# Kernel tuning notes

Hardware: AMD Instinct MI355X
Metric: run time of the kernel (lower is better)

## Reference

```python
import jax, jax.numpy as jnp
import numpy as np

T, B, E, H = 64, 64, 128, 256
N_ITEMS, N_DATA = 50000, 20000
EPS = 1e-8


def setup_inputs() -> dict:
    key = jax.random.key(0)
    ks = jax.random.split(key, 20)
    lengths = jnp.sort(jax.random.randint(ks[0], (B,), 1, T + 1))[::-1]
    lengths = lengths.at[0].set(T)  # pack_padded_sequence expects max length first
    x = jax.random.randint(ks[1], (T, B), 1, N_ITEMS)
    tmask = jnp.arange(T)[:, None] < lengths[None, :]
    x = jnp.where(tmask, x, 0)  # padding index 0
    s = 0.05
    emb_table = (jax.random.normal(ks[2], (N_ITEMS, E)) * s).at[0].set(0.0)  # padding_idx=0
    data_embeddings = jax.random.normal(ks[3], (N_DATA, E)) * s
    return {
        'x': x, 'lengths': lengths,
        'emb_table': emb_table, 'data_embeddings': data_embeddings,
        'W_ih': jax.random.normal(ks[4], (4 * H, E)) * s,
        'W_hh': jax.random.normal(ks[5], (4 * H, H)) * s,
        'b_ih': jax.random.normal(ks[6], (4 * H,)) * s,
        'b_hh': jax.random.normal(ks[7], (4 * H,)) * s,
        'Wq': jax.random.normal(ks[8], (H, H)) * s, 'bq': jax.random.normal(ks[9], (H,)) * s,
        'Wk': jax.random.normal(ks[10], (H, H)) * s, 'bk': jax.random.normal(ks[11], (H,)) * s,
        'Wv': jax.random.normal(ks[12], (H, H)) * s, 'bv': jax.random.normal(ks[13], (H,)) * s,
        'W_out': jax.random.normal(ks[14], (E, H)) * s, 'b_out': jax.random.normal(ks[15], (E,)) * s,
    }


def _forward(x, lengths, emb_table, data_embeddings, W_ih, W_hh, b_ih, b_hh,
             Wq, bq, Wk, bk, Wv, bv, W_out, b_out):
    t_len, b_sz = x.shape
    e_dim = emb_table.shape[1]
    h_dim = W_hh.shape[1]

    embs0 = emb_table[x]  # (T, B, E); dropout is identity in eval mode
    initial_embs = jax.lax.stop_gradient(embs0)  # .clone().detach() in original

    # PositionalEncoding: original slices by x.size(1) == batch dim (faithful quirk)
    pos = jnp.arange(b_sz, dtype=jnp.float32)[:, None]
    div = jnp.exp(jnp.arange(0, e_dim, 2, dtype=jnp.float32) * (-jnp.log(10000.0) / e_dim))
    enc = jnp.stack([jnp.sin(pos * div), jnp.cos(pos * div)], axis=-1).reshape(b_sz, e_dim)
    embs = embs0 + enc[None, :, :]  # broadcast over time

    # single-layer LSTM over time (gate order i, f, g, o)
    def step(carry, x_t):
        h, c = carry
        gates = x_t @ W_ih.T + h @ W_hh.T + (b_ih + b_hh)  # (B, 4H)
        i, f, g, o = jnp.split(gates, 4, axis=-1)
        c = jax.nn.sigmoid(f) * c + jax.nn.sigmoid(i) * jnp.tanh(g)
        h = jax.nn.sigmoid(o) * jnp.tanh(c)
        return (h, c), h

    h0 = jnp.zeros((b_sz, h_dim), embs.dtype)
    (_, _), lstm_out = jax.lax.scan(step, (h0, h0), embs)  # (T, B, H)

    # pack/pad round-trip zeroes outputs past each length (LSTM is causal)
    tmask = jnp.arange(t_len)[:, None] < lengths[None, :]  # (T, B)
    lstm_out = lstm_out * tmask[:, :, None]
    lstm_out = lstm_out.transpose(1, 0, 2)  # (B, T, H)

    padding_mask = jnp.sum(lstm_out, axis=-1) != 0  # (B, T)

    q = lstm_out @ Wq.T + bq
    k = lstm_out @ Wk.T + bk
    v = lstm_out @ Wv.T + bv
    score = jnp.einsum('bth,bsh->bts', q, k) / jnp.sqrt(jnp.float32(h_dim))
    score = jnp.where(padding_mask[:, None, :], score, -jnp.inf)
    attn = jax.nn.softmax(score, axis=2)
    weighted = jnp.einsum('bts,bsh->bth', attn, v)  # (B, T, H)
    attn_output = jnp.mean(weighted, axis=1) @ W_out.T + b_out  # (B, E)

    # kNN: fused normalize + matmul + argmin + gather over all T at once
    qn = initial_embs / jnp.clip(jnp.linalg.norm(initial_embs, axis=-1, keepdims=True), EPS)
    dn = data_embeddings / jnp.clip(jnp.linalg.norm(data_embeddings, axis=-1, keepdims=True), EPS)
    sims = jnp.einsum('tbe,ne->tbn', qn, dn)  # (T, B, N_DATA)
    idx = jnp.argmax(sims, axis=-1)  # argmin of (1 - sim)
    closest = jnp.mean(data_embeddings[idx], axis=0)  # (B, E)

    attn_output = attn_output * closest
    return attn_output @ emb_table.T  # (B, n_items)


def reference(x, lengths, emb_table, data_embeddings, W_ih, W_hh, b_ih, b_hh,
              Wq, bq, Wk, bk, Wv, bv, W_out, b_out):
    return _forward(x, lengths, emb_table, data_embeddings, W_ih, W_hh, b_ih, b_hh,
                    Wq, bq, Wk, bk, Wv, bv, W_out, b_out)
```

## Files before the change

### kernel.cpp

```cpp
#include <hip/hip_runtime.h>

typedef unsigned int uint;
typedef unsigned short ushort;
typedef unsigned long long u64;

#define NITEMS 50000
#define NDATA  20000
#define BLKCAP 4096u
#define OVCAP  65536u

#define OFF_LSTMOUT   0x0000000ULL
#define OFF_HX        0x0400000ULL
#define OFF_HXM       0x0440000ULL
#define OFF_PACKED    0x0480000ULL
#define OFF_PACKED2   0x0488000ULL
#define OFF_HITCNTS   0x0490000ULL
#define OFF_OHITCNT   0x0490800ULL
#define MEMSET_BYTES  0x0491000ULL
#define OFF_QMARGIN   0x0491000ULL
#define OFF_XW        0x05A0000ULL
#define OFF_QKV       0x15A0000ULL
#define OFF_HITBUF    OFF_QKV
#define OFF_WIHT      0x21A0000ULL
#define OFF_WQKVT     0x2220000ULL
#define OFF_BIASIH    0x22E0000ULL
#define OFF_BQKV      0x22E1000ULL
#define OFF_DNSCALE   0x22E2000ULL
#define OFF_AV        0x22FE000ULL
#define OFF_DEMB16    0x2306000ULL
#define OFF_A16       0x27E8000ULL
#define OFF_OVF       0x28E8000ULL

__device__ __forceinline__ ushort f2bf(float f) {
  union { float f; uint u; } v; v.f = f;
  uint u = v.u;
  return (ushort)((u + 0x7FFFu + ((u >> 16) & 1u)) >> 16);
}
__device__ __forceinline__ uint fkey(float f) {
  union { float f; uint u; } v; v.f = f;
  return (v.u & 0x80000000u) ? ~v.u : (v.u | 0x80000000u);
}
__device__ __forceinline__ u64 shfl_xor_u64(u64 v, int off) {
  uint lo = (uint)v, hi = (uint)(v >> 32);
  lo = (uint)__shfl_xor((int)lo, off);
  hi = (uint)__shfl_xor((int)hi, off);
  return ((u64)hi << 32) | (u64)lo;
}

typedef __attribute__((ext_vector_type(8))) short short8;
typedef __attribute__((ext_vector_type(4))) float floatx4;

#define R32(M) M(0) M(1) M(2) M(3) M(4) M(5) M(6) M(7) M(8) M(9) M(10) M(11) \
  M(12) M(13) M(14) M(15) M(16) M(17) M(18) M(19) M(20) M(21) M(22) M(23) \
  M(24) M(25) M(26) M(27) M(28) M(29) M(30) M(31)

#define HIX(j) ((j) + (((j) >> 7) << 2))

#define LBAR() do { \
  __builtin_amdgcn_sched_barrier(0); \
  asm volatile("s_waitcnt lgkmcnt(0)" ::: "memory"); \
  __builtin_amdgcn_s_barrier(); \
  __builtin_amdgcn_sched_barrier(0); \
} while (0)

__global__ __launch_bounds__(256) void prep_kernel(
    const int* __restrict__ x,
    const float* __restrict__ emb, const float* __restrict__ demb,
    const float* __restrict__ W_ih,
    const float* __restrict__ Wq, const float* __restrict__ Wk, const float* __restrict__ Wv,
    const float* __restrict__ b_ih, const float* __restrict__ b_hh,
    const float* __restrict__ bq, const float* __restrict__ bk, const float* __restrict__ bv,
    float* __restrict__ dnscale, ushort* __restrict__ demb16, ushort* __restrict__ a16,
    float* __restrict__ wiht, float* __restrict__ wqkvt,
    float* __restrict__ biasih, float* __restrict__ bqkv,
    float* __restrict__ qmargin, u64* __restrict__ packed2)
{
  int blk = blockIdx.x, tid = threadIdx.x;
  if (blk < 5000) {
    int row = blk * 4 + (tid >> 6);
    int lane = tid & 63;
    float2 d = *(const float2*)(demb + (size_t)row * 128 + lane * 2);
    float s = d.x * d.x + d.y * d.y;
    for (int off = 32; off; off >>= 1) s += __shfl_xor(s, off);
    if (lane == 0) dnscale[row] = 1.0f / fmaxf(sqrtf(s), 1e-8f);
  } else if (blk < 6250) {
    size_t base = ((size_t)(blk - 5000) * 256 + tid) * 8;
    float4 f1 = *(const float4*)(demb + base);
    float4 f2 = *(const float4*)(demb + base + 4);
    uint4 o;
    o.x = (uint)f2bf(f1.x) | ((uint)f2bf(f1.y) << 16);
    o.y = (uint)f2bf(f1.z) | ((uint)f2bf(f1.w) << 16);
    o.z = (uint)f2bf(f2.x) | ((uint)f2bf(f2.y) << 16);
    o.w = (uint)f2bf(f2.z) | ((uint)f2bf(f2.w) << 16);
    *(uint4*)(demb16 + base) = o;
  } else if (blk < 6506) {
    int idx = (blk - 6250) * 256 + tid;
    int m = idx >> 4, seg = idx & 15;
    const float* src = emb + (size_t)x[m] * 128 + seg * 8;
    float4 f1 = *(const float4*)(src);
    float4 f2 = *(const float4*)(src + 4);
    uint4 o;
    o.x = (uint)f2bf(f1.x) | ((uint)f2bf(f1.y) << 16);
    o.y = (uint)f2bf(f1.z) | ((uint)f2bf(f1.w) << 16);
    o.z = (uint)f2bf(f2.x) | ((uint)f2bf(f2.y) << 16);
    o.w = (uint)f2bf(f2.z) | ((uint)f2bf(f2.w) << 16);
    *(uint4*)(a16 + (size_t)m * 128 + seg * 8) = o;
  } else if (blk < 7018) {
    int f = (blk - 6506) * 256 + tid;
    int r = f >> 7, e = f & 127;
    wiht[e * 1024 + r] = W_ih[f];
  } else if (blk < 7786) {
    int f = (blk - 7018) * 256 + tid;
    int w = f >> 16; int rem = f & 65535;
    int r = rem >> 8, e = rem & 255;
    const float* src = (w == 0) ? Wq : (w == 1) ? Wk : Wv;
    wqkvt[e * 768 + w * 256 + r] = src[rem];
  } else if (blk < 7790) {
    int idx = (blk - 7786) * 256 + tid;
    if (idx < 1024) biasih[idx] = b_ih[idx] + b_hh[idx];
  } else if (blk < 7793) {
    int idx = (blk - 7790) * 256 + tid;
    if (idx < 768) {
      int w = idx >> 8; int r = idx & 255;
      const float* src = (w == 0) ? bq : (w == 1) ? bk : bv;
      bqkv[idx] = src[r];
    }
  } else {
    int row = (blk - 7793) * 4 + (tid >> 6);
    int lane = tid & 63;
    float2 d = *(const float2*)(emb + (size_t)x[row] * 128 + lane * 2);
    float s = d.x * d.x + d.y * d.y;
    for (int off = 32; off; off >>= 1) s += __shfl_xor(s, off);
    if (lane == 0) {
      if (s == 0.f) {
        qmargin[row] = -1e30f;
        packed2[row] = ((u64)fkey(0.0f) << 32) | 0xFFFFFFFFull;
      } else {
        qmargin[row] = 0.017f * sqrtf(s) + 1e-5f;
      }
    }
  }
}

__global__ __launch_bounds__(256) void xw_kernel(
    const int* __restrict__ x, const float* __restrict__ emb,
    const float* __restrict__ wiht, const float* __restrict__ biasih,
    float* __restrict__ xW)
{
  __shared__ __align__(16) float At[128 * 16];
  int blk = blockIdx.x, tid = threadIdx.x;
  int m0 = blk * 16;
  for (int c = 0; c < 8; ++c) {
    int idx = c * 256 + tid;
    int mm = idx >> 7, e = idx & 127;
    int m = m0 + mm;
    int bcol = m & 63;
    int xv = x[m];
    float val = emb[(size_t)xv * 128 + e];
    int j = e >> 1;
    float arg = (float)bcol * __expf((float)j * -0.14391157f);
    val += (e & 1) ? cosf(arg) : sinf(arg);
    At[e * 16 + mm] = val;
  }
  __syncthreads();
  int quad = tid >> 6, l = tid & 63;
  for (int rp = 0; rp < 4; ++rp) {
    int r = rp * 256 + l * 4;
    float acc[4][4] = {};
    for (int e = 0; e < 128; ++e) {
      float4 wv4 = *(const float4*)(wiht + e * 1024 + r);
      float4 av4 = *(const float4*)(At + e * 16 + quad * 4);
      float am[4] = {av4.x, av4.y, av4.z, av4.w};
      float wr4[4] = {wv4.x, wv4.y, wv4.z, wv4.w};
      #pragma unroll
      for (int mi = 0; mi < 4; ++mi)
        #pragma unroll
        for (int ri = 0; ri < 4; ++ri)
          acc[mi][ri] += am[mi] * wr4[ri];
    }
    float4 bv4 = *(const float4*)(biasih + r);
    #pragma unroll
    for (int mi = 0; mi < 4; ++mi) {
      size_t m = (size_t)(m0 + quad * 4 + mi);
      float4 o;
      o.x = acc[mi][0] + bv4.x; o.y = acc[mi][1] + bv4.y;
      o.z = acc[mi][2] + bv4.z; o.w = acc[mi][3] + bv4.w;
      *(float4*)(xW + m * 1024 + r) = o;
    }
  }
}

__global__ __launch_bounds__(512, 2) void lstm_knn_kernel(
    const int* __restrict__ lengths, const float* __restrict__ Whh,
    const float* __restrict__ xW, float* __restrict__ lstm_out,
    u64* __restrict__ hx, u64* __restrict__ hxm,
    const ushort* __restrict__ a16, const ushort* __restrict__ demb16,
    const float* __restrict__ dnscale, const float* __restrict__ qmargin,
    u64* __restrict__ packed, uint* __restrict__ hitcnts, uint* __restrict__ ohitcnt,
    uint* __restrict__ hitbuf, uint* __restrict__ ovbuf,
    const int* __restrict__ x, const float* __restrict__ emb,
    const float* __restrict__ demb, u64* __restrict__ packed2)
{
  __shared__ __align__(16) float h_sh[264];
  __shared__ float part_sh[256];
  __shared__ __align__(16) ushort b_sh[2][64 * 144];
  __shared__ uint lcnt;
  int tid = threadIdx.x;

  if (blockIdx.x < 256) {
    int blk = blockIdx.x;
    int b = blk & 63, q = blk >> 6;
    int row_local = tid >> 1, half = tid & 1;
    int gate = row_local >> 6, jloc = row_local & 63;
    int grow = gate * 256 + q * 64 + jloc;
    const float4* wp4 = (const float4*)(Whh + (size_t)grow * 256 + half * 128);
#define WDECL(i) float4 tt##i = wp4[i]; \
  float w##i##x = tt##i.x, w##i##y = tt##i.y, w##i##z = tt##i.z, w##i##w = tt##i.w;
    R32(WDECL)
#define WPIN(i) asm volatile("" : "+v"(w##i##x), "+v"(w##i##y), "+v"(w##i##z), "+v"(w##i##w));
    R32(WPIN)
    int len = lengths[b];
    if (tid < 256) h_sh[HIX(tid)] = 0.f;
    float cval = 0.f;
    int prm = tid - 320;
    int jr = (prm < q * 64) ? prm : prm + 64;
    bool fast_ok = true;
    int j1 = q * 64 + (tid - 64);
    float xw0 = 0.f, xw1 = 0.f, xw2 = 0.f, xw3 = 0.f;
    if (tid < 64) {
      const float* xwrow = xW + ((size_t)0 * 64 + b) * 1024 + q * 64 + tid;
      xw0 = xwrow[0]; xw1 = xwrow[256]; xw2 = xwrow[512]; xw3 = xwrow[768];
    }
    __syncthreads();
    for (int t = 0; t < len; ++t) {
      float nx0 = 0.f, nx1 = 0.f, nx2 = 0.f, nx3 = 0.f;
      if (tid < 64 && t + 1 < len) {
        const float* xwrow = xW + ((size_t)(t + 1) * 64 + b) * 1024 + q * 64 + tid;
        nx0 = xwrow[0]; nx1 = xwrow[256]; nx2 = xwrow[512]; nx3 = xwrow[768];
      }
      float hprev = 0.f;
      if (tid >= 64 && tid < 128 && t > 0) hprev = h_sh[HIX(j1)];
      const float4* h4 = (const float4*)(h_sh + half * 132);
      float a[4] = {0.f, 0.f, 0.f, 0.f};
#define WACC(i) { float4 hv_ = h4[i]; \
    a[(i) & 3] += w##i##x * hv_.x + w##i##y * hv_.y + w##i##z * hv_.z + w##i##w * hv_.w; }
      R32(WACC)
      float acc = (a[0] + a[2]) + (a[1] + a[3]);
      acc += __shfl_xor(acc, 1);
      if (!half) part_sh[row_local] = acc;
      LBAR();
      if (tid < 64) {
        float gi = part_sh[tid]       + xw0;
        float gf = part_sh[64 + tid]  + xw1;
        float gg = part_sh[128 + tid] + xw2;
        float go = part_sh[192 + tid] + xw3;
        float ii = 1.f / (1.f + __expf(-gi));
        float ff = 1.f / (1.f + __expf(-gf));
        float oo = 1.f / (1.f + __expf(-go));
        float tg = 1.f - 2.f / (1.f + __expf(2.f * gg));
        cval = ff * cval + ii * tg;
        float tc = 1.f - 2.f / (1.f + __expf(2.f * cval));
        float hv = oo * tc;
        int j = q * 64 + tid;
        union { float f; uint u; } cu; cu.f = hv;
        u64 pk = ((u64)cu.u << 32) | (u64)(uint)(t + 1);
        size_t slot = ((size_t)((t + 1) & 1) * 64 + b) * 256 + j;
        __builtin_amdgcn_sched_barrier(0);
        asm volatile("s_waitcnt vmcnt(4)" ::: "memory");
        asm volatile("global_store_dwordx2 %0, %1, off"
                     :: "v"(hxm + slot), "v"(pk) : "memory");
        __hip_atomic_store(hx + slot, pk, __ATOMIC_RELAXED, __HIP_MEMORY_SCOPE_AGENT);
        h_sh[HIX(j)] = hv;
        xw0 = nx0; xw1 = nx1; xw2 = nx2; xw3 = nx3;
      } else if (tid < 128) {
        if (t > 0) lstm_out[((size_t)b * 64 + (t - 1)) * 256 + j1] = hprev;
      } else if (tid >= 320 && t + 1 < len) {
        size_t slot = ((size_t)((t + 1) & 1) * 64 + b) * 256 + jr;
        uint want = (uint)(t + 1);
        u64 v = 0;
        bool got = false;
        if (fast_ok) {
          const u64* ms = hxm + slot;
          for (int tries = 0; tries < 32; ++tries) {
            asm volatile("global_load_dwordx2 %0, %1, off sc0\n\t"
                         "s_waitcnt vmcnt(0)"
                         : "=&v"(v) : "v"(ms) : "memory");
            if ((uint)v == want) { got = true; break; }
          }
          if (!got && t > 0) fast_ok = false;
        }
        if (!got) {
          const u64* as = hx + slot;
          int guard = 0;
          while (true) {
            v = __hip_atomic_load(as, __ATOMIC_RELAXED, __HIP_MEMORY_SCOPE_AGENT);
            if ((uint)v == want || ++guard > (1 << 24)) break;
          }
        }
        union { uint u; float f; } cv; cv.u = (uint)(v >> 32);
        h_sh[HIX(jr)] = cv.f;
      }
      LBAR();
    }
    if (tid >= 64 && tid < 128) {
      float hl = h_sh[HIX(j1)];
      lstm_out[((size_t)b * 64 + (len - 1)) * 256 + j1] = hl;
    }
    return;
  }

  int kb = blockIdx.x - 256;
  int chunk = kb & 15, mt = kb >> 4;
  int w8 = tid >> 6;
  int s = w8 >> 2, wv2 = w8 & 3;
  int lane = tid & 63;
  int col = lane & 15, quad = lane >> 4;
  int M0 = mt * 128;
  if (tid == 0) lcnt = 0;
  short8 afrag[4];
  {
    int mrow = M0 + s * 64 + wv2 * 16 + col;
    #pragma unroll
    for (int kf = 0; kf < 4; ++kf)
      afrag[kf] = *(const short8*)(a16 + (size_t)mrow * 128 + kf * 32 + quad * 8);
  }
  float best[4] = {-1e30f, -1e30f, -1e30f, -1e30f};
  int bidx[4] = {};
  int nbase = chunk * 1250, nend = nbase + 1250;
  const int niter = 20;
  int srow = tid >> 4, sseg = tid & 15;
  uint4 stg[2]; float scr[4];

  #pragma unroll
  for (int p = 0; p < 2; ++p) {
    int n = nbase + p * 32 + srow;
    uint4 v = {0u,0u,0u,0u};
    if (n < nend) v = *(const uint4*)(demb16 + (size_t)n * 128 + sseg * 8);
    stg[p] = v;
  }
  #pragma unroll
  for (int ns = 0; ns < 4; ++ns) {
    int n = nbase + ns * 16 + col;
    scr[ns] = (n < nend) ? dnscale[n] : 0.f;
  }
  for (int it = 0; it < niter; ++it) {
    int n0 = nbase + it * 64;
    ushort* bsh = b_sh[it & 1];
    #pragma unroll
    for (int p = 0; p < 2; ++p)
      *(uint4*)(&bsh[(p * 32 + srow) * 144 + sseg * 8]) = stg[p];
    float mysc[4] = {scr[0], scr[1], scr[2], scr[3]};
    __syncthreads();
    if (it + 1 < niter) {
      int nb = n0 + 64;
      #pragma unroll
      for (int p = 0; p < 2; ++p) {
        int n = nb + p * 32 + srow;
        uint4 v = {0u,0u,0u,0u};
        if (n < nend) v = *(const uint4*)(demb16 + (size_t)n * 128 + sseg * 8);
        stg[p] = v;
      }
      #pragma unroll
      for (int ns = 0; ns < 4; ++ns) {
        int n = nb + ns * 16 + col;
        scr[ns] = (n < nend) ? dnscale[n] : 0.f;
      }
    }
    #pragma unroll
    for (int ns = 0; ns < 4; ++ns) {
      short8 bfr[4];
      #pragma unroll
      for (int kf = 0; kf < 4; ++kf)
        bfr[kf] = *(const short8*)(&bsh[(ns * 16 + col) * 144 + kf * 32 + quad * 8]);
      int n = n0 + ns * 16 + col;
      float sc = mysc[ns];
      bool valid = (n < nend);
      floatx4 acc = {0.f, 0.f, 0.f, 0.f};
      #pragma unroll
      for (int kf = 0; kf < 4; ++kf)
        acc = __builtin_amdgcn_mfma_f32_16x16x32_bf16(afrag[kf], bfr[kf], acc, 0, 0, 0);
      #pragma unroll
      for (int r = 0; r < 4; ++r) {
        float sim = acc[r] * sc;
        if (valid && sim > best[r]) { best[r] = sim; bidx[r] = n; }
      }
    }
  }
  float thr[4];
  #pragma unroll
  for (int r = 0; r < 4; ++r) {
    u64 p = ((u64)fkey(best[r]) << 32) | (u64)(0xFFFFFFFFu - (uint)bidx[r]);
    #pragma unroll
    for (int off = 1; off < 16; off <<= 1) {
      u64 o = shfl_xor_u64(p, off);
      if (o > p) p = o;
    }
    int m = M0 + s * 64 + wv2 * 16 + quad * 4 + r;
    union { uint u; float f; } bu;
    uint k = (uint)(p >> 32);
    bu.u = (k & 0x80000000u) ? (k & 0x7FFFFFFFu) : ~k;
    thr[r] = bu.f - qmargin[m];
    if (col == 0)
      atomicMax((unsigned long long*)&packed[m], (unsigned long long)p);
  }
  __syncthreads();

  uint* myregion = hitbuf + (size_t)kb * BLKCAP;
  uint* ovregion = ovbuf;
  #pragma unroll
  for (int p = 0; p < 2; ++p) {
    int n = nbase + p * 32 + srow;
    uint4 v = {0u,0u,0u,0u};
    if (n < nend) v = *(const uint4*)(demb16 + (size_t)n * 128 + sseg * 8);
    stg[p] = v;
  }
  #pragma unroll
  for (int ns = 0; ns < 4; ++ns) {
    int n = nbase + ns * 16 + col;
    scr[ns] = (n < nend) ? dnscale[n] : 0.f;
  }
  for (int it = 0; it < niter; ++it) {
    int n0 = nbase + it * 64;
    ushort* bsh = b_sh[it & 1];
    #pragma unroll
    for (int p = 0; p < 2; ++p)
      *(uint4*)(&bsh[(p * 32 + srow) * 144 + sseg * 8]) = stg[p];
    float mysc[4] = {scr[0], scr[1], scr[2], scr[3]};
    __syncthreads();
    if (it + 1 < niter) {
      int nb = n0 + 64;
      #pragma unroll
      for (int p = 0; p < 2; ++p) {
        int n = nb + p * 32 + srow;
        uint4 v = {0u,0u,0u,0u};
        if (n < nend) v = *(const uint4*)(demb16 + (size_t)n * 128 + sseg * 8);
        stg[p] = v;
      }
      #pragma unroll
      for (int ns = 0; ns < 4; ++ns) {
        int n = nb + ns * 16 + col;
        scr[ns] = (n < nend) ? dnscale[n] : 0.f;
      }
    }
    #pragma unroll
    for (int ns = 0; ns < 4; ++ns) {
      short8 bfr[4];
      #pragma unroll
      for (int kf = 0; kf < 4; ++kf)
        bfr[kf] = *(const short8*)(&bsh[(ns * 16 + col) * 144 + kf * 32 + quad * 8]);
      int n = n0 + ns * 16 + col;
      float sc = mysc[ns];
      bool valid = (n < nend);
      floatx4 acc = {0.f, 0.f, 0.f, 0.f};
      #pragma unroll
      for (int kf = 0; kf < 4; ++kf)
        acc = __builtin_amdgcn_mfma_f32_16x16x32_bf16(afrag[kf], bfr[kf], acc, 0, 0, 0);
      #pragma unroll
      for (int r = 0; r < 4; ++r) {
        float sim = acc[r] * sc;
        bool hit = valid && (sim >= thr[r]);
        u64 mask = __ballot(hit);
        if (mask) {
          uint lcntv = (uint)__popcll(mask);
          int leader = __ffsll((unsigned long long)mask) - 1;
          uint base = 0;
          if (lane == leader) base = atomicAdd(&lcnt, lcntv);
          base = (uint)__shfl((int)base, leader);
          if (hit) {
            uint pos = base + (uint)__popcll(mask & ((1ull << lane) - 1ull));
            uint mm = (uint)(M0 + s * 64 + wv2 * 16 + quad * 4 + r);
            uint rec = (mm << 15) | (uint)n;
            if (pos < BLKCAP) {
              myregion[pos] = rec;
            } else {
              uint op = atomicAdd(ohitcnt, 1u);
              if (op < OVCAP) ovregion[op] = rec;
            }
          }
        }
      }
    }
  }
  __syncthreads();
  if (tid == 0) hitcnts[kb] = lcnt;
  uint rcnt = lcnt; if (rcnt > BLKCAP) rcnt = BLKCAP;
  for (uint h = tid; h < rcnt; h += 512) {
    uint rec = myregion[h];
    uint m = rec >> 15, n = rec & 0x7FFFu;
    if (m >= 4096 || n >= NDATA) continue;
    const float* qr = emb + (size_t)x[m] * 128;
    const float* dr = demb + (size_t)n * 128;
    double p = 0.0;
    #pragma unroll 8
    for (int e = 0; e < 128; e += 2) {
      float2 qv = *(const float2*)(qr + e);
      float2 dv = *(const float2*)(dr + e);
      p += (double)qv.x * (double)dv.x + (double)qv.y * (double)dv.y;
    }
    float sx = (float)(p * (double)dnscale[n]);
    u64 key = ((u64)fkey(sx) << 32) | (u64)(0xFFFFFFFFu - n);
    atomicMax((unsigned long long*)&packed2[m], (unsigned long long)key);
  }
}

__global__ __launch_bounds__(256) void fused_post_kernel(
    const float* __restrict__ lstm_out, const float* __restrict__ wqkvt,
    const float* __restrict__ bqkv, float* __restrict__ qkv,
    const u64* __restrict__ packed, const uint* __restrict__ ohitcnt,
    const uint* __restrict__ ovbuf, const int* __restrict__ x,
    const float* __restrict__ emb, const float* __restrict__ demb,
    const float* __restrict__ dnscale, u64* __restrict__ packed2)
{
  __shared__ __align__(16) float At[256 * 16];
  int blk = blockIdx.x, tid = threadIdx.x;
  if (blk < 256) {
    int m0 = blk * 16;
    for (int c = 0; c < 16; ++c)
      At[tid * 16 + c] = lstm_out[((size_t)m0 + c) * 256 + tid];
    __syncthreads();
    int quad = tid >> 6, l = tid & 63;
    for (int rp = 0; rp < 3; ++rp) {
      int r = rp * 256 + l * 4;
      float acc[4][4] = {};
      for (int e = 0; e < 256; ++e) {
        float4 wv4 = *(const float4*)(wqkvt + (size_t)e * 768 + r);
        float4 av4 = *(const float4*)(At + e * 16 + quad * 4);
        float am[4] = {av4.x, av4.y, av4.z, av4.w};
        float wr4[4] = {wv4.x, wv4.y, wv4.z, wv4.w};
        #pragma unroll
        for (int mi = 0; mi < 4; ++mi)
          #pragma unroll
          for (int ri = 0; ri < 4; ++ri)
            acc[mi][ri] += am[mi] * wr4[ri];
      }
      float4 bv4 = *(const float4*)(bqkv + r);
      #pragma unroll
      for (int mi = 0; mi < 4; ++mi) {
        size_t m = (size_t)(m0 + quad * 4 + mi);
        float4 o;
        o.x = acc[mi][0] + bv4.x; o.y = acc[mi][1] + bv4.y;
        o.z = acc[mi][2] + bv4.z; o.w = acc[mi][3] + bv4.w;
        *(float4*)(qkv + m * 768 + r) = o;
      }
    }
    return;
  }
  if (blk < 272) {
    uint m = (uint)(blk - 256) * 256 + tid;
    uint n = 0xFFFFFFFFu - (uint)(packed[m] & 0xFFFFFFFFull);
    if (n < NDATA) {
      const float* qr = emb + (size_t)x[m] * 128;
      const float* dr = demb + (size_t)n * 128;
      double p = 0.0;
      #pragma unroll 8
      for (int e = 0; e < 128; e += 2) {
        float2 qv = *(const float2*)(qr + e);
        float2 dv = *(const float2*)(dr + e);
        p += (double)qv.x * (double)dv.x + (double)qv.y * (double)dv.y;
      }
      float sx = (float)(p * (double)dnscale[n]);
      u64 key = ((u64)fkey(sx) << 32) | (u64)(0xFFFFFFFFu - n);
      atomicMax((unsigned long long*)&packed2[m], (unsigned long long)key);
    }
    return;
  }
  uint cnt = *ohitcnt; if (cnt > OVCAP) cnt = OVCAP;
  for (uint h = (uint)(blk - 272) * 256 + tid; h < cnt; h += 16 * 256) {
    uint rec = ovbuf[h];
    uint m = rec >> 15, n = rec & 0x7FFFu;
    if (m >= 4096 || n >= NDATA) continue;
    const float* qr = emb + (size_t)x[m] * 128;
    const float* dr = demb + (size_t)n * 128;
    double p = 0.0;
    #pragma unroll 8
    for (int e = 0; e < 128; e += 2) {
      float2 qv = *(const float2*)(qr + e);
      float2 dv = *(const float2*)(dr + e);
      p += (double)qv.x * (double)dv.x + (double)qv.y * (double)dv.y;
    }
    float sx = (float)(p * (double)dnscale[n]);
    u64 key = ((u64)fkey(sx) << 32) | (u64)(0xFFFFFFFFu - n);
    atomicMax((unsigned long long*)&packed2[m], (unsigned long long)key);
  }
}

__global__ __launch_bounds__(256) void attn_kernel(
    const float* __restrict__ qkv, const int* __restrict__ lengths,
    const u64* __restrict__ packed2, const float* __restrict__ demb,
    const float* __restrict__ W_out, const float* __restrict__ b_out,
    float* __restrict__ av)
{
  __shared__ float k_sh[64 * 257];
  __shared__ __align__(16) float q_sh[4 * 256];
  __shared__ float wpart[4 * 64];
  __shared__ float wtot[64];
  __shared__ float out_sh[256];
  int b = blockIdx.x, tid = threadIdx.x;
  int wv = tid >> 6, lane = tid & 63;
  int len = lengths[b];
  for (int s = 0; s < 64; ++s)
    k_sh[s * 257 + tid] = qkv[((size_t)b * 64 + s) * 768 + 256 + tid];
  float clv = 0.f;
  if (tid < 128) {
    float sum = 0.f;
    for (int t = 0; t < 64; ++t) {
      uint low = (uint)(packed2[t * 64 + b] & 0xFFFFFFFFull);
      uint n = 0xFFFFFFFFu - low;
      if (n >= NDATA) n = 0;
      sum += demb[(size_t)n * 128 + tid];
    }
    clv = sum * (1.0f / 64.0f);
  }
  wpart[tid] = 0.f;
  for (int tq = 0; tq < 16; ++tq) {
    __syncthreads();
    #pragma unroll
    for (int c = 0; c < 4; ++c)
      q_sh[c * 256 + tid] = qkv[((size_t)b * 64 + tq * 4 + c) * 768 + tid];
    __syncthreads();
    const float* krow = k_sh + lane * 257;
    const float* qrow = q_sh + wv * 256;
    float sc = 0.f;
    #pragma unroll 8
    for (int h = 0; h < 256; ++h)
      sc += qrow[h] * krow[h];
    sc *= 0.0625f;
    bool vs = (lane < len);
    float scm = vs ? sc : -1e30f;
    float mx = scm;
    for (int off = 32; off; off >>= 1) mx = fmaxf(mx, __shfl_xor(mx, off));
    float e = vs ? __expf(sc - mx) : 0.f;
    float sum = e;
    for (int off = 32; off; off >>= 1) sum += __shfl_xor(sum, off);
    wpart[wv * 64 + lane] += e / sum;
  }
  __syncthreads();
  if (tid < 64)
    wtot[tid] = (wpart[tid] + wpart[64 + tid] + wpart[128 + tid] + wpart[192 + tid]) * (1.0f / 64.0f);
  __syncthreads();
  {
    float acc = 0.f;
    for (int s = 0; s < 64; ++s)
      acc += wtot[s] * qkv[((size_t)b * 64 + s) * 768 + 512 + tid];
    out_sh[tid] = acc;
  }
  __syncthreads();
  if (tid < 128) {
    const float4* wr = (const float4*)(W_out + (size_t)tid * 256);
    float p = b_out[tid];
    #pragma unroll
    for (int c = 0; c < 64; ++c) {
      float4 u = wr[c];
      p += out_sh[c * 4 + 0] * u.x + out_sh[c * 4 + 1] * u.y
         + out_sh[c * 4 + 2] * u.z + out_sh[c * 4 + 3] * u.w;
    }
    av[tid * 64 + b] = p * clv;
  }
}

__global__ __launch_bounds__(256) void final_kernel(
    const float* __restrict__ emb, const float* __restrict__ av,
    float* __restrict__ out)
{
  int i = blockIdx.x * 256 + threadIdx.x;
  if (i >= NITEMS) return;
  const float4* row = (const float4*)(emb + (size_t)i * 128);
  float acc[64];
  #pragma unroll
  for (int bb = 0; bb < 64; ++bb) acc[bb] = 0.f;
  for (int e4 = 0; e4 < 32; ++e4) {
    float4 u = row[e4];
    float wvv[4] = {u.x, u.y, u.z, u.w};
    const float* ab = av + e4 * 4 * 64;
    #pragma unroll
    for (int j = 0; j < 4; ++j) {
      #pragma unroll
      for (int bb = 0; bb < 64; ++bb)
        acc[bb] += wvv[j] * ab[j * 64 + bb];
    }
  }
  #pragma unroll
  for (int bb = 0; bb < 64; ++bb)
    out[(size_t)bb * NITEMS + i] = acc[bb];
}

extern "C" void kernel_launch(void* const* d_in, const int* in_sizes, int n_in,
                              void* d_out, int out_size, void* d_ws, size_t ws_size,
                              hipStream_t stream)
{
  const int*   x       = (const int*)d_in[0];
  const int*   lengths = (const int*)d_in[1];
  const float* emb     = (const float*)d_in[2];
  const float* demb    = (const float*)d_in[3];
  const float* W_ih    = (const float*)d_in[4];
  const float* W_hh    = (const float*)d_in[5];
  const float* b_ih    = (const float*)d_in[6];
  const float* b_hh    = (const float*)d_in[7];
  const float* Wq      = (const float*)d_in[8];
  const float* bq      = (const float*)d_in[9];
  const float* Wk      = (const float*)d_in[10];
  const float* bk      = (const float*)d_in[11];
  const float* Wv      = (const float*)d_in[12];
  const float* bv      = (const float*)d_in[13];
  const float* W_out   = (const float*)d_in[14];
  const float* b_out   = (const float*)d_in[15];

  char* ws = (char*)d_ws;
  float*  lstm_out = (float*)(ws + OFF_LSTMOUT);
  u64*    hx       = (u64*)(ws + OFF_HX);
  u64*    hxm      = (u64*)(ws + OFF_HXM);
  u64*    packed   = (u64*)(ws + OFF_PACKED);
  u64*    packed2  = (u64*)(ws + OFF_PACKED2);
  uint*   hitcnts  = (uint*)(ws + OFF_HITCNTS);
  uint*   ohitcnt  = (uint*)(ws + OFF_OHITCNT);
  float*  qmargin  = (float*)(ws + OFF_QMARGIN);
  uint*   hitbuf   = (uint*)(ws + OFF_HITBUF);
  uint*   ovbuf    = (uint*)(ws + OFF_OVF);
  float*  xW       = (float*)(ws + OFF_XW);
  float*  qkv      = (float*)(ws + OFF_QKV);
  float*  wiht     = (float*)(ws + OFF_WIHT);
  float*  wqkvt    = (float*)(ws + OFF_WQKVT);
  float*  biasih   = (float*)(ws + OFF_BIASIH);
  float*  bqkv     = (float*)(ws + OFF_BQKV);
  float*  dnscale  = (float*)(ws + OFF_DNSCALE);
  float*  av       = (float*)(ws + OFF_AV);
  ushort* demb16   = (ushort*)(ws + OFF_DEMB16);
  ushort* a16      = (ushort*)(ws + OFF_A16);

  hipMemsetAsync(d_ws, 0, (size_t)MEMSET_BYTES, stream);

  hipLaunchKernelGGL(prep_kernel, dim3(8817), dim3(256), 0, stream,
                     x, emb, demb, W_ih, Wq, Wk, Wv, b_ih, b_hh, bq, bk, bv,
                     dnscale, demb16, a16, wiht, wqkvt, biasih, bqkv,
                     qmargin, packed2);
  hipLaunchKernelGGL(xw_kernel, dim3(256), dim3(256), 0, stream,
                     x, emb, wiht, biasih, xW);
  hipLaunchKernelGGL(lstm_knn_kernel, dim3(768), dim3(512), 0, stream,
                     lengths, W_hh, xW, lstm_out, hx, hxm,
                     a16, demb16, dnscale, qmargin, packed, hitcnts, ohitcnt,
                     hitbuf, ovbuf, x, emb, demb, packed2);
  hipLaunchKernelGGL(fused_post_kernel, dim3(288), dim3(256), 0, stream,
                     lstm_out, wqkvt, bqkv, qkv, packed, ohitcnt, ovbuf,
                     x, emb, demb, dnscale, packed2);
  hipLaunchKernelGGL(attn_kernel, dim3(64), dim3(256), 0, stream,
                     qkv, lengths, packed2, demb, W_out, b_out, av);
  hipLaunchKernelGGL(final_kernel, dim3(196), dim3(256), 0, stream,
                     emb, av, (float*)d_out);
}
```

Baseline: 587.2 us.

## Double kNN M-tile per block to reuse staged data tiles across two query slabs

```diff
diff --git a/kernel.cpp b/kernel.cpp
--- a/kernel.cpp
+++ b/kernel.cpp
@@ -312,20 +312,20 @@
   int kb = blockIdx.x - 256;
   int chunk = kb & 15, mt = kb >> 4;
   int w8 = tid >> 6;
-  int s = w8 >> 2, wv2 = w8 & 3;
   int lane = tid & 63;
   int col = lane & 15, quad = lane >> 4;
-  int M0 = mt * 128;
+  int M0 = mt * 256;
   if (tid == 0) lcnt = 0;
-  short8 afrag[4];
-  {
-    int mrow = M0 + s * 64 + wv2 * 16 + col;
+  short8 afrag[2][4];
+  #pragma unroll
+  for (int s = 0; s < 2; ++s) {
+    int mrow = M0 + s * 128 + w8 * 16 + col;
     #pragma unroll
     for (int kf = 0; kf < 4; ++kf)
-      afrag[kf] = *(const short8*)(a16 + (size_t)mrow * 128 + kf * 32 + quad * 8);
-  }
-  float best[4] = {-1e30f, -1e30f, -1e30f, -1e30f};
-  int bidx[4] = {};
+      afrag[s][kf] = *(const short8*)(a16 + (size_t)mrow * 128 + kf * 32 + quad * 8);
+  }
+  float best[2][4] = {{-1e30f,-1e30f,-1e30f,-1e30f},{-1e30f,-1e30f,-1e30f,-1e30f}};
+  int bidx[2][4] = {};
   int nbase = chunk * 1250, nend = nbase + 1250;
   const int niter = 20;
   int srow = tid >> 4, sseg = tid & 15;
@@ -375,34 +375,39 @@
       int n = n0 + ns * 16 + col;
       float sc = mysc[ns];
       bool valid = (n < nend);
-      floatx4 acc = {0.f, 0.f, 0.f, 0.f};
-      #pragma unroll
-      for (int kf = 0; kf < 4; ++kf)
-        acc = __builtin_amdgcn_mfma_f32_16x16x32_bf16(afrag[kf], bfr[kf], acc, 0, 0, 0);
-      #pragma unroll
-      for (int r = 0; r < 4; ++r) {
-        float sim = acc[r] * sc;
-        if (valid && sim > best[r]) { best[r] = sim; bidx[r] = n; }
-      }
-    }
-  }
-  float thr[4];
+      #pragma unroll
+      for (int s = 0; s < 2; ++s) {
+        floatx4 acc = {0.f, 0.f, 0.f, 0.f};
+        #pragma unroll
+        for (int kf = 0; kf < 4; ++kf)
+          acc = __builtin_amdgcn_mfma_f32_16x16x32_bf16(afrag[s][kf], bfr[kf], acc, 0, 0, 0);
+        #pragma unroll
+        for (int r = 0; r < 4; ++r) {
+          float sim = acc[r] * sc;
+          if (valid && sim > best[s][r]) { best[s][r] = sim; bidx[s][r] = n; }
+        }
+      }
+    }
+  }
+  float thr[2][4];
   #pragma unroll
-  for (int r = 0; r < 4; ++r) {
-    u64 p = ((u64)fkey(best[r]) << 32) | (u64)(0xFFFFFFFFu - (uint)bidx[r]);
-    #pragma unroll
-    for (int off = 1; off < 16; off <<= 1) {
-      u64 o = shfl_xor_u64(p, off);
-      if (o > p) p = o;
-    }
-    int m = M0 + s * 64 + wv2 * 16 + quad * 4 + r;
-    union { uint u; float f; } bu;
-    uint k = (uint)(p >> 32);
-    bu.u = (k & 0x80000000u) ? (k & 0x7FFFFFFFu) : ~k;
-    thr[r] = bu.f - qmargin[m];
-    if (col == 0)
-      atomicMax((unsigned long long*)&packed[m], (unsigned long long)p);
-  }
+  for (int s = 0; s < 2; ++s)
+    #pragma unroll
+    for (int r = 0; r < 4; ++r) {
+      u64 p = ((u64)fkey(best[s][r]) << 32) | (u64)(0xFFFFFFFFu - (uint)bidx[s][r]);
+      #pragma unroll
+      for (int off = 1; off < 16; off <<= 1) {
+        u64 o = shfl_xor_u64(p, off);
+        if (o > p) p = o;
+      }
+      int m = M0 + s * 128 + w8 * 16 + quad * 4 + r;
+      union { uint u; float f; } bu;
+      uint k = (uint)(p >> 32);
+      bu.u = (k & 0x80000000u) ? (k & 0x7FFFFFFFu) : ~k;
+      thr[s][r] = bu.f - qmargin[m];
+      if (col == 0)
+        atomicMax((unsigned long long*)&packed[m], (unsigned long long)p);
+    }
   __syncthreads();
 
   uint* myregion = hitbuf + (size_t)kb * BLKCAP;
@@ -451,30 +456,33 @@
       int n = n0 + ns * 16 + col;
       float sc = mysc[ns];
       bool valid = (n < nend);
-      floatx4 acc = {0.f, 0.f, 0.f, 0.f};
-      #pragma unroll
-      for (int kf = 0; kf < 4; ++kf)
-        acc = __builtin_amdgcn_mfma_f32_16x16x32_bf16(afrag[kf], bfr[kf], acc, 0, 0, 0);
-      #pragma unroll
-      for (int r = 0; r < 4; ++r) {
-        float sim = acc[r] * sc;
-        bool hit = valid && (sim >= thr[r]);
-        u64 mask = __ballot(hit);
-        if (mask) {
-          uint lcntv = (uint)__popcll(mask);
-          int leader = __ffsll((unsigned long long)mask) - 1;
-          uint base = 0;
-          if (lane == leader) base = atomicAdd(&lcnt, lcntv);
-          base = (uint)__shfl((int)base, leader);
-          if (hit) {
-            uint pos = base + (uint)__popcll(mask & ((1ull << lane) - 1ull));
-            uint mm = (uint)(M0 + s * 64 + wv2 * 16 + quad * 4 + r);
-            uint rec = (mm << 15) | (uint)n;
-            if (pos < BLKCAP) {
-              myregion[pos] = rec;
-            } else {
-              uint op = atomicAdd(ohitcnt, 1u);
-              if (op < OVCAP) ovregion[op] = rec;
+      #pragma unroll
+      for (int s = 0; s < 2; ++s) {
+        floatx4 acc = {0.f, 0.f, 0.f, 0.f};
+        #pragma unroll
+        for (int kf = 0; kf < 4; ++kf)
+          acc = __builtin_amdgcn_mfma_f32_16x16x32_bf16(afrag[s][kf], bfr[kf], acc, 0, 0, 0);
+        #pragma unroll
+        for (int r = 0; r < 4; ++r) {
+          float sim = acc[r] * sc;
+          bool hit = valid && (sim >= thr[s][r]);
+          u64 mask = __ballot(hit);
+          if (mask) {
+            uint lcntv = (uint)__popcll(mask);
+            int leader = __ffsll((unsigned long long)mask) - 1;
+            uint base = 0;
+            if (lane == leader) base = atomicAdd(&lcnt, lcntv);
+            base = (uint)__shfl((int)base, leader);
+            if (hit) {
+              uint pos = base + (uint)__popcll(mask & ((1ull << lane) - 1ull));
+              uint mm = (uint)(M0 + s * 128 + w8 * 16 + quad * 4 + r);
+              uint rec = (mm << 15) | (uint)n;
+              if (pos < BLKCAP) {
+                myregion[pos] = rec;
+              } else {
+                uint op = atomicAdd(ohitcnt, 1u);
+                if (op < OVCAP) ovregion[op] = rec;
+              }
             }
           }
         }
@@ -735,7 +743,7 @@
                      qmargin, packed2);
   hipLaunchKernelGGL(xw_kernel, dim3(256), dim3(256), 0, stream,
                      x, emb, wiht, biasih, xW);
-  hipLaunchKernelGGL(lstm_knn_kernel, dim3(768), dim3(512), 0, stream,
+  hipLaunchKernelGGL(lstm_knn_kernel, dim3(512), dim3(512), 0, stream,
                      lengths, W_hh, xW, lstm_out, hx, hxm,
                      a16, demb16, dnscale, qmargin, packed, hitcnts, ohitcnt,
                      hitbuf, ovbuf, x, emb, demb, packed2);
```

Result: no change. 577.9 us (-1.6%).
